# Optimization experiments

Hardware: AMD Instinct MI355X
Metric: run time of the kernel (lower is better)

The kernel has to match this reference:

```python
import jax, jax.numpy as jnp
import numpy as np

# 5-tap binomial kernel, same as torch module
_H5 = jnp.array([0.0625, 0.25, 0.375, 0.25, 0.0625], dtype=jnp.float32)
_K1 = _H5[:, None] * _H5[None, :]        # 5x5 Gaussian, sums to 1 (reduce kernel)
_K4 = 4.0 * _K1                           # expand kernel (gain 4)
# polyphase sub-kernels for expand (match torch strided slicing of kernel)
_KER00 = _K4[0::2, 0::2]  # 3x3
_KER01 = _K4[0::2, 1::2]  # 3x2
_KER10 = _K4[1::2, 0::2]  # 2x3
_KER11 = _K4[1::2, 1::2]  # 2x2


def _dwconv(x, k, stride=1):
    """Depthwise valid conv, same kernel per channel. x: NCHW, k: (kh, kw)."""
    C = x.shape[1]
    kern = jnp.broadcast_to(k[None, None].astype(x.dtype), (C, 1) + k.shape)
    return jax.lax.conv_general_dilated(
        x, kern, (stride, stride), 'VALID',
        dimension_numbers=('NCHW', 'OIHW', 'NCHW'),
        feature_group_count=C)


def pyr_reduce(im):
    # replicate-pad 2 each side, 5x5 conv, subsample [0::2,0::2] == stride-2 conv
    x = jnp.pad(im, ((0, 0), (0, 0), (2, 2), (2, 2)), mode='edge')
    return _dwconv(x, _K1, stride=2)


def pyr_expand(im):
    B, C, H, W = im.shape
    x_r2c2 = jnp.pad(im, ((0, 0), (0, 0), (1, 1), (1, 1)), mode='edge')  # top+bot, left+right
    x_r2c1 = jnp.pad(im, ((0, 0), (0, 0), (1, 1), (0, 1)), mode='edge')  # top+bot, right
    x_c2r1 = jnp.pad(im, ((0, 0), (0, 0), (0, 1), (1, 1)), mode='edge')  # bot, left+right
    x_c1r1 = jnp.pad(im, ((0, 0), (0, 0), (0, 1), (0, 1)), mode='edge')  # bot, right
    o00 = _dwconv(x_r2c2, _KER00)  # -> out[0::2, 0::2]
    o01 = _dwconv(x_r2c1, _KER01)  # -> out[0::2, 1::2]
    o10 = _dwconv(x_c2r1, _KER10)  # -> out[1::2, 0::2]
    o11 = _dwconv(x_c1r1, _KER11)  # -> out[1::2, 1::2]
    out = jnp.zeros((B, C, 2 * H, 2 * W), im.dtype)
    out = out.at[:, :, 0::2, 0::2].set(o00)
    out = out.at[:, :, 0::2, 1::2].set(o01)
    out = out.at[:, :, 1::2, 0::2].set(o10)
    out = out.at[:, :, 1::2, 1::2].set(o11)
    return out


def setup_inputs() -> dict:
    key = jax.random.key(0)
    im = jax.random.normal(key, (16, 3, 1024, 1024), dtype=jnp.float32)
    return {"im": im, "levels": 5}


def reference(im, levels):
    gpyr = [im]
    for _ in range(levels - 1):
        gpyr.append(pyr_reduce(gpyr[-1]))
    lpyr = [gpyr[l] - pyr_expand(gpyr[l + 1]) for l in range(levels - 1)]
    lpyr.append(gpyr[-1])
    return tuple(lpyr)
```

## Files before the change

### kernel.cpp

```cpp
#include <hip/hip_runtime.h>


#define RBX 64
#define RBY 4

template <bool EDGE>
__device__ __forceinline__ void reduce_accum(const float* __restrict__ src,
                                             int Hin, int Win, int rbase, int cb,
                                             float (&acc)[4][4]) {
    const float w0 = 0.0625f, w1 = 0.25f, w2 = 0.375f;
    const float wr[5] = {w0, w1, w2, w1, w0};
#pragma unroll
    for (int rr = 0; rr < 11; ++rr) {
        int gr = rbase + rr;
        gr = gr < 0 ? 0 : (gr > Hin - 1 ? Hin - 1 : gr);
        const float* row = src + (size_t)gr * Win;
        float v[16];
        if (!EDGE) {
#pragma unroll
            for (int q = 0; q < 4; ++q) {
                float4 f = *reinterpret_cast<const float4*>(row + cb + 4 * q);
                v[4 * q + 0] = f.x; v[4 * q + 1] = f.y;
                v[4 * q + 2] = f.z; v[4 * q + 3] = f.w;
            }
        } else {
#pragma unroll
            for (int c = 0; c < 16; ++c) {
                int gc = cb + c;
                gc = gc < 0 ? 0 : (gc > Win - 1 ? Win - 1 : gc);
                v[c] = row[gc];
            }
        }
        float h[4];
#pragma unroll
        for (int c = 0; c < 4; ++c) {
            const float* vv = v + 2 + 2 * c;
            float s04 = vv[0] + vv[4];
            float s13 = vv[1] + vv[3];
            float hh = w0 * s04;
            hh = fmaf(w1, s13, hh);
            hh = fmaf(w2, vv[2], hh);
            h[c] = hh;
        }
#pragma unroll
        for (int i = 0; i < 4; ++i) {
            const int a = rr - 2 * i;
            if (a >= 0 && a <= 4) {
                const float w = wr[a];
#pragma unroll
                for (int c = 0; c < 4; ++c)
                    acc[i][c] = fmaf(w, h[c], acc[i][c]);
            }
        }
    }
}

__launch_bounds__(256)
__global__ void reduce_kernel(const float* __restrict__ in, float* __restrict__ out,
                              int Hin, int Win, int Hout, int Wout) {
    const int p = blockIdx.z;
    const int t = blockIdx.x * RBX + threadIdx.x;
    const int i0 = (blockIdx.y * RBY + threadIdx.y) * 4;
    const int j0 = 4 * t;
    if (j0 >= Wout || i0 >= Hout) return;

    const float* src = in + (size_t)p * Hin * Win;
    const int cb = 8 * t - 4;
    const int rbase = 2 * i0 - 2;
    const bool edge = (cb < 0) | (cb + 15 > Win - 1);

    float acc[4][4];
#pragma unroll
    for (int i = 0; i < 4; ++i)
#pragma unroll
        for (int c = 0; c < 4; ++c) acc[i][c] = 0.f;

    if (!edge) reduce_accum<false>(src, Hin, Win, rbase, cb, acc);
    else       reduce_accum<true>(src, Hin, Win, rbase, cb, acc);

    float* drow = out + (size_t)p * Hout * Wout + j0;
#pragma unroll
    for (int i = 0; i < 4; ++i) {
        *reinterpret_cast<float4*>(drow + (size_t)(i0 + i) * Wout) =
            make_float4(acc[i][0], acc[i][1], acc[i][2], acc[i][3]);
    }
}

__launch_bounds__(256)
__global__ void lap_kernel(const float* __restrict__ fine, const float* __restrict__ coarse,
                           float* __restrict__ out, int Hc, int Wc) {
    const int t = blockIdx.x * blockDim.x + threadIdx.x;
    const int i = blockIdx.y * blockDim.y + threadIdx.y;
    const int p = blockIdx.z;
    const int Wc2 = Wc >> 1;
    if (i >= Hc || t >= Wc2) return;

    const float* g = coarse + (size_t)p * Hc * Wc;
    const int im1 = i > 0 ? i - 1 : 0;
    const int ip1 = i < Hc - 1 ? i + 1 : Hc - 1;
    const float* rm = g + (size_t)im1 * Wc;
    const float* r0 = g + (size_t)i   * Wc;
    const float* rp = g + (size_t)ip1 * Wc;

    const int jl = 2 * t - 1 > 0 ? 2 * t - 1 : 0;
    const int jr = 2 * t + 2 < Wc - 1 ? 2 * t + 2 : Wc - 1;

    float cm[4], c0[4], cp[4];
    {
        float2 m = *(const float2*)(rm + 2 * t);
        float2 z = *(const float2*)(r0 + 2 * t);
        float2 q = *(const float2*)(rp + 2 * t);
        cm[1] = m.x; cm[2] = m.y;
        c0[1] = z.x; c0[2] = z.y;
        cp[1] = q.x; cp[2] = q.y;
        cm[0] = rm[jl]; cm[3] = rm[jr];
        c0[0] = r0[jl]; c0[3] = r0[jr];
        cp[0] = rp[jl]; cp[3] = rp[jr];
    }

    float e[4], o[4];
#pragma unroll
    for (int c = 0; c < 4; ++c) {
        e[c] = fmaf(0.125f, cm[c], fmaf(0.75f, c0[c], 0.125f * cp[c]));
        o[c] = 0.5f * (c0[c] + cp[c]);
    }

    float ev0 = fmaf(0.125f, e[0], fmaf(0.75f, e[1], 0.125f * e[2]));
    float ev1 = 0.5f * (e[1] + e[2]);
    float ev2 = fmaf(0.125f, e[1], fmaf(0.75f, e[2], 0.125f * e[3]));
    float ev3 = 0.5f * (e[2] + e[3]);
    float od0 = fmaf(0.125f, o[0], fmaf(0.75f, o[1], 0.125f * o[2]));
    float od1 = 0.5f * (o[1] + o[2]);
    float od2 = fmaf(0.125f, o[1], fmaf(0.75f, o[2], 0.125f * o[3]));
    float od3 = 0.5f * (o[2] + o[3]);

    const int Wf = 2 * Wc;
    const size_t fbase = (size_t)p * (size_t)(2 * Hc) * Wf;
    const float4* f0 = (const float4*)(fine + fbase + (size_t)(2 * i) * Wf);
    const float4* f1 = (const float4*)(fine + fbase + (size_t)(2 * i + 1) * Wf);
    float4 a = f0[t], b = f1[t];

    float4* w0p = (float4*)(out + fbase + (size_t)(2 * i) * Wf);
    float4* w1p = (float4*)(out + fbase + (size_t)(2 * i + 1) * Wf);
    w0p[t] = make_float4(a.x - ev0, a.y - ev1, a.z - ev2, a.w - ev3);
    w1p[t] = make_float4(b.x - od0, b.y - od1, b.z - od2, b.w - od3);
}

extern "C" void kernel_launch(void* const* d_in, const int* in_sizes, int n_in,
                              void* d_out, int out_size, void* d_ws, size_t ws_size,
                              hipStream_t stream) {
    (void)in_sizes; (void)n_in; (void)d_ws; (void)ws_size; (void)out_size;
    const float* im = (const float*)d_in[0];
    float* out = (float*)d_out;

    const int P = 48;
    const int H0 = 1024, W0 = 1024;

    size_t off[5];
    size_t acc = 0;
    for (int l = 0; l < 5; ++l) {
        off[l] = acc;
        int h = H0 >> l, w = W0 >> l;
        acc += (size_t)P * h * w;
    }

    for (int l = 0; l < 4; ++l) {
        int Hin = H0 >> l, Win = W0 >> l;
        int Hout = Hin >> 1, Wout = Win >> 1;
        const float* src = (l == 0) ? im : (out + off[l]);
        float* dst = out + off[l + 1];
        dim3 blk(RBX, RBY, 1);
        dim3 grid((Wout + 4 * RBX - 1) / (4 * RBX), (Hout + 4 * RBY - 1) / (4 * RBY), P);
        reduce_kernel<<<grid, blk, 0, stream>>>(src, dst, Hin, Win, Hout, Wout);
    }

    for (int l = 0; l < 4; ++l) {
        int Hc = H0 >> (l + 1), Wc = W0 >> (l + 1);
        const float* fine = (l == 0) ? im : (out + off[l]);
        const float* coarse = out + off[l + 1];
        float* dst = out + off[l];
        dim3 blk(64, 4, 1);
        dim3 grid((Wc / 2 + 63) / 64, (Hc + 3) / 4, P);
        lap_kernel<<<grid, blk, 0, stream>>>(fine, coarse, dst, Hc, Wc);
    }
}
```

Before: 507.7 us.

## Fuse Laplacian level with next reduce in one launch, widen lap per-thread work

Merges each Laplacian level's expand-subtract with the next Gaussian reduce into a single launch, split by blockIdx.y ranges. This cuts the number of kernel launches and lets independent work overlap. The Laplacian kernel now produces eight output columns per thread instead of four. The first level uses nontemporal loads and stores for the large fine image. The risks are wasted idle blocks, since the fused grid's x-dimension is the max of both parts, and the fine-image load width changes with the wider per-thread work.

```diff
diff --git a/kernel.cpp b/kernel.cpp
--- a/kernel.cpp
+++ b/kernel.cpp
@@ -3,6 +3,8 @@
 
 #define RBX 64
 #define RBY 4
+
+typedef float fx4 __attribute__((ext_vector_type(4)));
 
 template <bool EDGE>
 __device__ __forceinline__ void reduce_accum(const float* __restrict__ src,
@@ -19,7 +21,7 @@
         if (!EDGE) {
 #pragma unroll
             for (int q = 0; q < 4; ++q) {
-                float4 f = *reinterpret_cast<const float4*>(row + cb + 4 * q);
+                fx4 f = *reinterpret_cast<const fx4*>(row + cb + 4 * q);
                 v[4 * q + 0] = f.x; v[4 * q + 1] = f.y;
                 v[4 * q + 2] = f.z; v[4 * q + 3] = f.w;
             }
@@ -55,95 +57,147 @@
     }
 }
 
+__device__ __forceinline__ void reduce_block(const float* __restrict__ src,
+                                             float* __restrict__ dst,
+                                             int Hin, int Win, int Hout, int Wout,
+                                             int bx, int by, int tx, int ty) {
+    const int t = bx * RBX + tx;
+    const int i0 = (by * RBY + ty) * 4;
+    const int j0 = 4 * t;
+    if (j0 >= Wout || i0 >= Hout) return;
+
+    const int cb = 8 * t - 4;
+    const int rbase = 2 * i0 - 2;
+    const bool edge = (cb < 0) | (cb + 15 > Win - 1);
+
+    float acc[4][4];
+#pragma unroll
+    for (int i = 0; i < 4; ++i)
+#pragma unroll
+        for (int c = 0; c < 4; ++c) acc[i][c] = 0.f;
+
+    if (!edge) reduce_accum<false>(src, Hin, Win, rbase, cb, acc);
+    else       reduce_accum<true>(src, Hin, Win, rbase, cb, acc);
+
+    float* drow = dst + j0;
+#pragma unroll
+    for (int i = 0; i < 4; ++i) {
+        fx4 o = {acc[i][0], acc[i][1], acc[i][2], acc[i][3]};
+        *reinterpret_cast<fx4*>(drow + (size_t)(i0 + i) * Wout) = o;
+    }
+}
+
 __launch_bounds__(256)
 __global__ void reduce_kernel(const float* __restrict__ in, float* __restrict__ out,
                               int Hin, int Win, int Hout, int Wout) {
     const int p = blockIdx.z;
-    const int t = blockIdx.x * RBX + threadIdx.x;
-    const int i0 = (blockIdx.y * RBY + threadIdx.y) * 4;
-    const int j0 = 4 * t;
-    if (j0 >= Wout || i0 >= Hout) return;
-
-    const float* src = in + (size_t)p * Hin * Win;
-    const int cb = 8 * t - 4;
-    const int rbase = 2 * i0 - 2;
-    const bool edge = (cb < 0) | (cb + 15 > Win - 1);
-
-    float acc[4][4];
-#pragma unroll
-    for (int i = 0; i < 4; ++i)
-#pragma unroll
-        for (int c = 0; c < 4; ++c) acc[i][c] = 0.f;
-
-    if (!edge) reduce_accum<false>(src, Hin, Win, rbase, cb, acc);
-    else       reduce_accum<true>(src, Hin, Win, rbase, cb, acc);
-
-    float* drow = out + (size_t)p * Hout * Wout + j0;
-#pragma unroll
-    for (int i = 0; i < 4; ++i) {
-        *reinterpret_cast<float4*>(drow + (size_t)(i0 + i) * Wout) =
-            make_float4(acc[i][0], acc[i][1], acc[i][2], acc[i][3]);
-    }
+    reduce_block(in + (size_t)p * Hin * Win, out + (size_t)p * Hout * Wout,
+                 Hin, Win, Hout, Wout, blockIdx.x, blockIdx.y, threadIdx.x, threadIdx.y);
+}
+
+template <bool NT>
+__device__ __forceinline__ fx4 ld4(const float* p) {
+    if (NT) return __builtin_nontemporal_load(reinterpret_cast<const fx4*>(p));
+    return *reinterpret_cast<const fx4*>(p);
+}
+template <bool NT>
+__device__ __forceinline__ void st4(float* p, fx4 v) {
+    if (NT) __builtin_nontemporal_store(v, reinterpret_cast<fx4*>(p));
+    else    *reinterpret_cast<fx4*>(p) = v;
+}
+
+template <bool NT>
+__device__ __forceinline__ void lap_block(const float* __restrict__ fine,
+                                          const float* __restrict__ coarse,
+                                          float* __restrict__ out,
+                                          int Hc, int Wc, int bx, int by, int tx, int ty) {
+    const int t = bx * 64 + tx;
+    const int i = by * 4 + ty;
+    if (i >= Hc || t >= (Wc >> 2)) return;
+
+    const int im1 = i > 0 ? i - 1 : 0;
+    const int ip1 = i < Hc - 1 ? i + 1 : Hc - 1;
+    const float* rm = coarse + (size_t)im1 * Wc;
+    const float* r0 = coarse + (size_t)i   * Wc;
+    const float* rp = coarse + (size_t)ip1 * Wc;
+
+    const int jl = 4 * t - 1 > 0 ? 4 * t - 1 : 0;
+    const int jr = 4 * t + 4 < Wc - 1 ? 4 * t + 4 : Wc - 1;
+
+    float cm[6], c0[6], cp[6];
+    {
+        fx4 m = *reinterpret_cast<const fx4*>(rm + 4 * t);
+        fx4 z = *reinterpret_cast<const fx4*>(r0 + 4 * t);
+        fx4 q = *reinterpret_cast<const fx4*>(rp + 4 * t);
+        cm[1] = m.x; cm[2] = m.y; cm[3] = m.z; cm[4] = m.w;
+        c0[1] = z.x; c0[2] = z.y; c0[3] = z.z; c0[4] = z.w;
+        cp[1] = q.x; cp[2] = q.y; cp[3] = q.z; cp[4] = q.w;
+        cm[0] = rm[jl]; cm[5] = rm[jr];
+        c0[0] = r0[jl]; c0[5] = r0[jr];
+        cp[0] = rp[jl]; cp[5] = rp[jr];
+    }
+
+    float e[6], o[6];
+#pragma unroll
+    for (int c = 0; c < 6; ++c) {
+        e[c] = fmaf(0.125f, cm[c], fmaf(0.75f, c0[c], 0.125f * cp[c]));
+        o[c] = 0.5f * (c0[c] + cp[c]);
+    }
+
+    float ev[8], ov[8];
+#pragma unroll
+    for (int q = 0; q < 4; ++q) {
+        ev[2 * q]     = fmaf(0.125f, e[q], fmaf(0.75f, e[q + 1], 0.125f * e[q + 2]));
+        ev[2 * q + 1] = 0.5f * (e[q + 1] + e[q + 2]);
+        ov[2 * q]     = fmaf(0.125f, o[q], fmaf(0.75f, o[q + 1], 0.125f * o[q + 2]));
+        ov[2 * q + 1] = 0.5f * (o[q + 1] + o[q + 2]);
+    }
+
+    const int Wf = 2 * Wc;
+    const size_t r0off = (size_t)(2 * i) * Wf + 8 * t;
+    const float* f0 = fine + r0off;
+    const float* f1 = f0 + Wf;
+    fx4 a0 = ld4<NT>(f0), a1 = ld4<NT>(f0 + 4);
+    fx4 b0 = ld4<NT>(f1), b1 = ld4<NT>(f1 + 4);
+
+    float* w0 = out + r0off;
+    float* w1 = w0 + Wf;
+    fx4 o0 = {a0.x - ev[0], a0.y - ev[1], a0.z - ev[2], a0.w - ev[3]};
+    fx4 o1 = {a1.x - ev[4], a1.y - ev[5], a1.z - ev[6], a1.w - ev[7]};
+    fx4 o2 = {b0.x - ov[0], b0.y - ov[1], b0.z - ov[2], b0.w - ov[3]};
+    fx4 o3 = {b1.x - ov[4], b1.y - ov[5], b1.z - ov[6], b1.w - ov[7]};
+    st4<NT>(w0,     o0);
+    st4<NT>(w0 + 4, o1);
+    st4<NT>(w1,     o2);
+    st4<NT>(w1 + 4, o3);
 }
 
 __launch_bounds__(256)
 __global__ void lap_kernel(const float* __restrict__ fine, const float* __restrict__ coarse,
                            float* __restrict__ out, int Hc, int Wc) {
-    const int t = blockIdx.x * blockDim.x + threadIdx.x;
-    const int i = blockIdx.y * blockDim.y + threadIdx.y;
     const int p = blockIdx.z;
-    const int Wc2 = Wc >> 1;
-    if (i >= Hc || t >= Wc2) return;
-
-    const float* g = coarse + (size_t)p * Hc * Wc;
-    const int im1 = i > 0 ? i - 1 : 0;
-    const int ip1 = i < Hc - 1 ? i + 1 : Hc - 1;
-    const float* rm = g + (size_t)im1 * Wc;
-    const float* r0 = g + (size_t)i   * Wc;
-    const float* rp = g + (size_t)ip1 * Wc;
-
-    const int jl = 2 * t - 1 > 0 ? 2 * t - 1 : 0;
-    const int jr = 2 * t + 2 < Wc - 1 ? 2 * t + 2 : Wc - 1;
-
-    float cm[4], c0[4], cp[4];
-    {
-        float2 m = *(const float2*)(rm + 2 * t);
-        float2 z = *(const float2*)(r0 + 2 * t);
-        float2 q = *(const float2*)(rp + 2 * t);
-        cm[1] = m.x; cm[2] = m.y;
-        c0[1] = z.x; c0[2] = z.y;
-        cp[1] = q.x; cp[2] = q.y;
-        cm[0] = rm[jl]; cm[3] = rm[jr];
-        c0[0] = r0[jl]; c0[3] = r0[jr];
-        cp[0] = rp[jl]; cp[3] = rp[jr];
-    }
-
-    float e[4], o[4];
-#pragma unroll
-    for (int c = 0; c < 4; ++c) {
-        e[c] = fmaf(0.125f, cm[c], fmaf(0.75f, c0[c], 0.125f * cp[c]));
-        o[c] = 0.5f * (c0[c] + cp[c]);
-    }
-
-    float ev0 = fmaf(0.125f, e[0], fmaf(0.75f, e[1], 0.125f * e[2]));
-    float ev1 = 0.5f * (e[1] + e[2]);
-    float ev2 = fmaf(0.125f, e[1], fmaf(0.75f, e[2], 0.125f * e[3]));
-    float ev3 = 0.5f * (e[2] + e[3]);
-    float od0 = fmaf(0.125f, o[0], fmaf(0.75f, o[1], 0.125f * o[2]));
-    float od1 = 0.5f * (o[1] + o[2]);
-    float od2 = fmaf(0.125f, o[1], fmaf(0.75f, o[2], 0.125f * o[3]));
-    float od3 = 0.5f * (o[2] + o[3]);
-
-    const int Wf = 2 * Wc;
-    const size_t fbase = (size_t)p * (size_t)(2 * Hc) * Wf;
-    const float4* f0 = (const float4*)(fine + fbase + (size_t)(2 * i) * Wf);
-    const float4* f1 = (const float4*)(fine + fbase + (size_t)(2 * i + 1) * Wf);
-    float4 a = f0[t], b = f1[t];
-
-    float4* w0p = (float4*)(out + fbase + (size_t)(2 * i) * Wf);
-    float4* w1p = (float4*)(out + fbase + (size_t)(2 * i + 1) * Wf);
-    w0p[t] = make_float4(a.x - ev0, a.y - ev1, a.z - ev2, a.w - ev3);
-    w1p[t] = make_float4(b.x - od0, b.y - od1, b.z - od2, b.w - od3);
+    const size_t mplane = (size_t)Hc * Wc;
+    lap_block<false>(fine + (size_t)p * 4 * mplane, coarse + (size_t)p * mplane,
+                     out + (size_t)p * 4 * mplane, Hc, Wc,
+                     blockIdx.x, blockIdx.y, threadIdx.x, threadIdx.y);
+}
+
+template <bool NT>
+__launch_bounds__(256)
+__global__ void fused_kernel(const float* __restrict__ fine, const float* __restrict__ mid,
+                             float* __restrict__ lap_dst, float* __restrict__ red_dst,
+                             int Hc, int Wc, int ylap) {
+    const int p = blockIdx.z;
+    const size_t mplane = (size_t)Hc * Wc;
+    if ((int)blockIdx.y < ylap) {
+        lap_block<NT>(fine + (size_t)p * 4 * mplane, mid + (size_t)p * mplane,
+                      lap_dst + (size_t)p * 4 * mplane, Hc, Wc,
+                      blockIdx.x, blockIdx.y, threadIdx.x, threadIdx.y);
+    } else {
+        reduce_block(mid + (size_t)p * mplane, red_dst + (size_t)p * (mplane >> 2),
+                     Hc, Wc, Hc >> 1, Wc >> 1,
+                     blockIdx.x, (int)blockIdx.y - ylap, threadIdx.x, threadIdx.y);
+    }
 }
 
 extern "C" void kernel_launch(void* const* d_in, const int* in_sizes, int n_in,
@@ -164,23 +218,35 @@
         acc += (size_t)P * h * w;
     }
 
-    for (int l = 0; l < 4; ++l) {
-        int Hin = H0 >> l, Win = W0 >> l;
-        int Hout = Hin >> 1, Wout = Win >> 1;
-        const float* src = (l == 0) ? im : (out + off[l]);
-        float* dst = out + off[l + 1];
+    {
+        int Hout = H0 >> 1, Wout = W0 >> 1;
         dim3 blk(RBX, RBY, 1);
-        dim3 grid((Wout + 4 * RBX - 1) / (4 * RBX), (Hout + 4 * RBY - 1) / (4 * RBY), P);
-        reduce_kernel<<<grid, blk, 0, stream>>>(src, dst, Hin, Win, Hout, Wout);
-    }
-
-    for (int l = 0; l < 4; ++l) {
+        dim3 grid((Wout + 255) / 256, (Hout + 15) / 16, P);
+        reduce_kernel<<<grid, blk, 0, stream>>>(im, out + off[1], H0, W0, Hout, Wout);
+    }
+
+    for (int l = 0; l < 3; ++l) {
         int Hc = H0 >> (l + 1), Wc = W0 >> (l + 1);
+        int xlap = (Wc / 4 + 63) / 64, ylap = (Hc + 3) / 4;
+        int Hout = Hc >> 1, Wout = Wc >> 1;
+        int xred = (Wout + 255) / 256, yred = (Hout + 15) / 16;
+        dim3 blk(64, 4, 1);
+        dim3 grid(xlap > xred ? xlap : xred, ylap + yred, P);
         const float* fine = (l == 0) ? im : (out + off[l]);
-        const float* coarse = out + off[l + 1];
-        float* dst = out + off[l];
+        if (l == 0)
+            fused_kernel<true><<<grid, blk, 0, stream>>>(fine, out + off[l + 1],
+                                                         out + off[l], out + off[l + 2],
+                                                         Hc, Wc, ylap);
+        else
+            fused_kernel<false><<<grid, blk, 0, stream>>>(fine, out + off[l + 1],
+                                                          out + off[l], out + off[l + 2],
+                                                          Hc, Wc, ylap);
+    }
+
+    {
+        int Hc = H0 >> 4, Wc = W0 >> 4;
         dim3 blk(64, 4, 1);
-        dim3 grid((Wc / 2 + 63) / 64, (Hc + 3) / 4, P);
-        lap_kernel<<<grid, blk, 0, stream>>>(fine, coarse, dst, Hc, Wc);
-    }
-}
+        dim3 grid((Wc / 4 + 63) / 64, (Hc + 3) / 4, P);
+        lap_kernel<<<grid, blk, 0, stream>>>(out + off[3], out + off[4], out + off[3], Hc, Wc);
+    }
+}
```

Measured after the change: 487.6 us. -3.9%, faster.
